# Kernel tuning notes

Measured on AMD Instinct MI355X. Metric: run time of the kernel, lower is better.

Reference implementation:

```python
import jax, jax.numpy as jnp
import numpy as np

NUM_CLASSES = 19
IGNORE_INDEX = -1


def setup_inputs() -> dict:
    key = jax.random.key(0)
    k1, k2 = jax.random.split(key)
    pred_label = jax.random.normal(k1, (8, NUM_CLASSES, 512, 1024), dtype=jnp.float32)
    label = jax.random.randint(k2, (8, 512, 1024), 0, NUM_CLASSES, dtype=jnp.int64)
    return {"pred_label": pred_label, "label": label}


def reference(pred_label, label):
    # argmax over class dim -> [B, H, W]
    pred = jnp.argmax(pred_label, axis=1)
    p = pred.reshape(-1)
    l = label.reshape(-1)
    valid = (l != IGNORE_INDEX).astype(jnp.float32)
    # clip label so ignore entries index a real bin; their weight is zero anyway
    lc = jnp.clip(l, 0, NUM_CLASSES - 1)
    # batched bincounts replace the per-image histc loop: all images summed at once
    area_label = jnp.bincount(lc, weights=valid, length=NUM_CLASSES)
    area_pred = jnp.bincount(p, weights=valid, length=NUM_CLASSES)
    inter_w = valid * (p == l).astype(jnp.float32)
    area_intersect = jnp.bincount(lc, weights=inter_w, length=NUM_CLASSES)
    area_union = area_pred + area_label - area_intersect
    iou = area_intersect / area_union  # 0/0 -> nan, matching torch/numpy
    result = jnp.nanmean(iou)
    result = jnp.where(jnp.isnan(result), jnp.float32(0.5), result)
    return 1.0 - result
```

## Files before the change

### kernel.cpp

```cpp
#include <hip/hip_runtime.h>

#define NUM_CLASSES 19
#define IGNORE_INDEX (-1)
#define BATCH 8
#define HW (512 * 1024)
#define NPIX (BATCH * HW)
#define NGROUP (NPIX / 4)
#define NBINS (3 * NUM_CLASSES)
#define BINS_PAD 64
#define HBLOCKS 4096

__global__ __launch_bounds__(256) void iou_hist_kernel(
    const float* __restrict__ pred,
    const int* __restrict__ label,
    unsigned int* __restrict__ bh)
{
    __shared__ unsigned int h[4][NBINS];
    const int tid = threadIdx.x;
    const int wid = tid >> 6;

    for (int i = tid; i < 4 * NBINS; i += 256) ((unsigned int*)h)[i] = 0u;
    __syncthreads();

    unsigned int* __restrict__ hw_ = h[wid];

    const int g  = blockIdx.x * 256 + tid;
    const int p  = g << 2;
    const int b  = p >> 19;
    const int hw = p & (HW - 1);

    const float4* __restrict__ bp4 =
        (const float4*)(pred + (size_t)b * (size_t)(NUM_CLASSES * HW) + hw);

    float4 best = bp4[0];
    int bcx = 0, bcy = 0, bcz = 0, bcw = 0;
#pragma unroll
    for (int c = 1; c < NUM_CLASSES; ++c) {
        const float4 v = bp4[(size_t)c * (HW / 4)];
        if (v.x > best.x) { best.x = v.x; bcx = c; }
        if (v.y > best.y) { best.y = v.y; bcy = c; }
        if (v.z > best.z) { best.z = v.z; bcz = c; }
        if (v.w > best.w) { best.w = v.w; bcw = c; }
    }

    const int4 lab = ((const int4*)label)[g];

    {
        const int l = lab.x;
        if (l != IGNORE_INDEX) {
            const int lc = min(max(l, 0), NUM_CLASSES - 1);
            atomicAdd(&hw_[lc], 1u);
            atomicAdd(&hw_[NUM_CLASSES + bcx], 1u);
            if (bcx == l) atomicAdd(&hw_[2 * NUM_CLASSES + lc], 1u);
        }
    }
    {
        const int l = lab.y;
        if (l != IGNORE_INDEX) {
            const int lc = min(max(l, 0), NUM_CLASSES - 1);
            atomicAdd(&hw_[lc], 1u);
            atomicAdd(&hw_[NUM_CLASSES + bcy], 1u);
            if (bcy == l) atomicAdd(&hw_[2 * NUM_CLASSES + lc], 1u);
        }
    }
    {
        const int l = lab.z;
        if (l != IGNORE_INDEX) {
            const int lc = min(max(l, 0), NUM_CLASSES - 1);
            atomicAdd(&hw_[lc], 1u);
            atomicAdd(&hw_[NUM_CLASSES + bcz], 1u);
            if (bcz == l) atomicAdd(&hw_[2 * NUM_CLASSES + lc], 1u);
        }
    }
    {
        const int l = lab.w;
        if (l != IGNORE_INDEX) {
            const int lc = min(max(l, 0), NUM_CLASSES - 1);
            atomicAdd(&hw_[lc], 1u);
            atomicAdd(&hw_[NUM_CLASSES + bcw], 1u);
            if (bcw == l) atomicAdd(&hw_[2 * NUM_CLASSES + lc], 1u);
        }
    }

    __syncthreads();
    unsigned int* __restrict__ outp = bh + (size_t)blockIdx.x * BINS_PAD;
    for (int i = tid; i < BINS_PAD; i += 256) {
        const unsigned int s = (i < NBINS)
            ? (h[0][i] + h[1][i] + h[2][i] + h[3][i]) : 0u;
        outp[i] = s;
    }
}

__global__ __launch_bounds__(1024) void iou_finish_kernel(
    const unsigned int* __restrict__ bh, float* __restrict__ out)
{
    __shared__ unsigned int part[16][BINS_PAD];
    const int tid = threadIdx.x;
    const int bin = tid & 63;
    const int row = tid >> 6;

    unsigned int s = 0;
    for (int b = row; b < HBLOCKS; b += 16)
        s += bh[(size_t)b * BINS_PAD + bin];
    part[row][bin] = s;
    __syncthreads();

    if (tid < BINS_PAD) {
        unsigned int t = 0;
#pragma unroll
        for (int r = 0; r < 16; ++r) t += part[r][tid];
        part[0][tid] = t;
    }
    __syncthreads();

    if (tid == 0) {
        float sum = 0.0f;
        int cnt = 0;
        for (int c = 0; c < NUM_CLASSES; ++c) {
            const float a_lab = (float)part[0][c];
            const float a_prd = (float)part[0][NUM_CLASSES + c];
            const float a_int = (float)part[0][2 * NUM_CLASSES + c];
            const float a_uni = a_prd + a_lab - a_int;
            if (a_uni > 0.0f) { sum += a_int / a_uni; ++cnt; }
        }
        const float mean = (cnt > 0) ? (sum / (float)cnt) : 0.5f;
        out[0] = 1.0f - mean;
    }
}

extern "C" void kernel_launch(void* const* d_in, const int* in_sizes, int n_in,
                              void* d_out, int out_size, void* d_ws, size_t ws_size,
                              hipStream_t stream)
{
    const float* pred  = (const float*)d_in[0];
    const int*   label = (const int*)d_in[1];
    float*       out   = (float*)d_out;
    unsigned int* bh   = (unsigned int*)d_ws;

    iou_hist_kernel<<<HBLOCKS, 256, 0, stream>>>(pred, label, bh);
    iou_finish_kernel<<<1, 1024, 0, stream>>>(bh, out);
}
```

Measured before the change: 441.5 us.

## Use per-thread 16-bit LDS histograms instead of shared atomics; batch class loads

Each thread now owns a column in a 57x258 unsigned-short shared histogram and increments it without atomics, removing contention from shared-memory atomicAdd on only 19 bins per wave. At the end, 57 threads each reduce one row by reading packed 16-bit pairs. Each thread handles four pixel groups and issues all 19 class float4 loads before the argmax to raise memory-level parallelism, so the block count drops fourfold. The larger LDS footprint (about 29 KB per block) and higher register use may limit occupancy.

```diff
diff --git a/kernel.cpp b/kernel.cpp
--- a/kernel.cpp
+++ b/kernel.cpp
@@ -8,86 +8,103 @@
 #define NGROUP (NPIX / 4)
 #define NBINS (3 * NUM_CLASSES)
 #define BINS_PAD 64
-#define HBLOCKS 4096
+#define GPT 4
+#define THREADS 256
+#define HBLOCKS (NGROUP / (THREADS * GPT))
+#define PADC 258
 
-__global__ __launch_bounds__(256) void iou_hist_kernel(
+__global__ __launch_bounds__(THREADS) void iou_hist_kernel(
     const float* __restrict__ pred,
     const int* __restrict__ label,
     unsigned int* __restrict__ bh)
 {
-    __shared__ unsigned int h[4][NBINS];
+    __shared__ unsigned short h[NBINS][PADC];
     const int tid = threadIdx.x;
-    const int wid = tid >> 6;
 
-    for (int i = tid; i < 4 * NBINS; i += 256) ((unsigned int*)h)[i] = 0u;
+    {
+        unsigned int* h32 = (unsigned int*)&h[0][0];
+        for (int i = tid; i < (NBINS * PADC) / 2; i += THREADS) h32[i] = 0u;
+    }
     __syncthreads();
 
-    unsigned int* __restrict__ hw_ = h[wid];
+    const int gbase = blockIdx.x * (THREADS * GPT);
+    const int pbase = gbase << 2;
+    const int b   = pbase >> 19;
+    const int hw0 = pbase & (HW - 1);
+    const float4* __restrict__ p4 =
+        (const float4*)(pred + (size_t)b * (size_t)(NUM_CLASSES * HW) + hw0);
+    const int4* __restrict__ lab4 = (const int4*)label + gbase;
 
-    const int g  = blockIdx.x * 256 + tid;
-    const int p  = g << 2;
-    const int b  = p >> 19;
-    const int hw = p & (HW - 1);
+#pragma unroll
+    for (int i = 0; i < GPT; ++i) {
+        const int off = i * THREADS + tid;
 
-    const float4* __restrict__ bp4 =
-        (const float4*)(pred + (size_t)b * (size_t)(NUM_CLASSES * HW) + hw);
+        float4 v[NUM_CLASSES];
+#pragma unroll
+        for (int c = 0; c < NUM_CLASSES; ++c)
+            v[c] = p4[(size_t)c * (HW / 4) + off];
+        const int4 lab = lab4[off];
 
-    float4 best = bp4[0];
-    int bcx = 0, bcy = 0, bcz = 0, bcw = 0;
+        float4 best = v[0];
+        int bx = 0, by = 0, bz = 0, bw = 0;
 #pragma unroll
-    for (int c = 1; c < NUM_CLASSES; ++c) {
-        const float4 v = bp4[(size_t)c * (HW / 4)];
-        if (v.x > best.x) { best.x = v.x; bcx = c; }
-        if (v.y > best.y) { best.y = v.y; bcy = c; }
-        if (v.z > best.z) { best.z = v.z; bcz = c; }
-        if (v.w > best.w) { best.w = v.w; bcw = c; }
-    }
+        for (int c = 1; c < NUM_CLASSES; ++c) {
+            if (v[c].x > best.x) { best.x = v[c].x; bx = c; }
+            if (v[c].y > best.y) { best.y = v[c].y; by = c; }
+            if (v[c].z > best.z) { best.z = v[c].z; bz = c; }
+            if (v[c].w > best.w) { best.w = v[c].w; bw = c; }
+        }
 
-    const int4 lab = ((const int4*)label)[g];
-
-    {
-        const int l = lab.x;
-        if (l != IGNORE_INDEX) {
-            const int lc = min(max(l, 0), NUM_CLASSES - 1);
-            atomicAdd(&hw_[lc], 1u);
-            atomicAdd(&hw_[NUM_CLASSES + bcx], 1u);
-            if (bcx == l) atomicAdd(&hw_[2 * NUM_CLASSES + lc], 1u);
+        {
+            const int l = lab.x;
+            if (l != IGNORE_INDEX) {
+                const int lc = min(max(l, 0), NUM_CLASSES - 1);
+                h[lc][tid]++;
+                h[NUM_CLASSES + bx][tid]++;
+                if (bx == l) h[2 * NUM_CLASSES + lc][tid]++;
+            }
         }
-    }
-    {
-        const int l = lab.y;
-        if (l != IGNORE_INDEX) {
-            const int lc = min(max(l, 0), NUM_CLASSES - 1);
-            atomicAdd(&hw_[lc], 1u);
-            atomicAdd(&hw_[NUM_CLASSES + bcy], 1u);
-            if (bcy == l) atomicAdd(&hw_[2 * NUM_CLASSES + lc], 1u);
+        {
+            const int l = lab.y;
+            if (l != IGNORE_INDEX) {
+                const int lc = min(max(l, 0), NUM_CLASSES - 1);
+                h[lc][tid]++;
+                h[NUM_CLASSES + by][tid]++;
+                if (by == l) h[2 * NUM_CLASSES + lc][tid]++;
+            }
         }
-    }
-    {
-        const int l = lab.z;
-        if (l != IGNORE_INDEX) {
-            const int lc = min(max(l, 0), NUM_CLASSES - 1);
-            atomicAdd(&hw_[lc], 1u);
-            atomicAdd(&hw_[NUM_CLASSES + bcz], 1u);
-            if (bcz == l) atomicAdd(&hw_[2 * NUM_CLASSES + lc], 1u);
+        {
+            const int l = lab.z;
+            if (l != IGNORE_INDEX) {
+                const int lc = min(max(l, 0), NUM_CLASSES - 1);
+                h[lc][tid]++;
+                h[NUM_CLASSES + bz][tid]++;
+                if (bz == l) h[2 * NUM_CLASSES + lc][tid]++;
+            }
         }
-    }
-    {
-        const int l = lab.w;
-        if (l != IGNORE_INDEX) {
-            const int lc = min(max(l, 0), NUM_CLASSES - 1);
-            atomicAdd(&hw_[lc], 1u);
-            atomicAdd(&hw_[NUM_CLASSES + bcw], 1u);
-            if (bcw == l) atomicAdd(&hw_[2 * NUM_CLASSES + lc], 1u);
+        {
+            const int l = lab.w;
+            if (l != IGNORE_INDEX) {
+                const int lc = min(max(l, 0), NUM_CLASSES - 1);
+                h[lc][tid]++;
+                h[NUM_CLASSES + bw][tid]++;
+                if (bw == l) h[2 * NUM_CLASSES + lc][tid]++;
+            }
         }
     }
 
     __syncthreads();
-    unsigned int* __restrict__ outp = bh + (size_t)blockIdx.x * BINS_PAD;
-    for (int i = tid; i < BINS_PAD; i += 256) {
-        const unsigned int s = (i < NBINS)
-            ? (h[0][i] + h[1][i] + h[2][i] + h[3][i]) : 0u;
-        outp[i] = s;
+    if (tid < BINS_PAD) {
+        unsigned int s = 0u;
+        if (tid < NBINS) {
+            const unsigned int* row = (const unsigned int*)&h[tid][0];
+#pragma unroll 8
+            for (int i = 0; i < PADC / 2; ++i) {
+                const unsigned int u = row[i];
+                s += (u & 0xffffu) + (u >> 16);
+            }
+        }
+        bh[(size_t)blockIdx.x * BINS_PAD + tid] = s;
     }
 }
 
@@ -137,6 +154,6 @@
     float*       out   = (float*)d_out;
     unsigned int* bh   = (unsigned int*)d_ws;
 
-    iou_hist_kernel<<<HBLOCKS, 256, 0, stream>>>(pred, label, bh);
+    iou_hist_kernel<<<HBLOCKS, THREADS, 0, stream>>>(pred, label, bh);
     iou_finish_kernel<<<1, 1024, 0, stream>>>(bh, out);
 }
```

Result: no change. 438.9 us (-0.6%).
